# Optimization experiments

Hardware: AMD Instinct MI355X
Metric: run time of the kernel (lower is better)

The kernel has to match this reference:

```python
import jax, jax.numpy as jnp
import numpy as np
from jax import lax

WIN = 7
K1, K2 = 0.01, 0.03
NP_ = WIN * WIN
COV_NORM = NP_ / (NP_ - 1)


def _box_filter(t, w):
    # t: [B, C, H, W] -> valid 7x7 box mean, [B, C, H-6, W-6]
    B, C, H, W = t.shape
    o = lax.conv_general_dilated(
        t.reshape(B * C, 1, H, W), w, window_strides=(1, 1), padding='VALID',
        dimension_numbers=('NCHW', 'OIHW', 'NCHW'))
    return o.reshape(B, C, H - WIN + 1, W - WIN + 1)


def setup_inputs() -> dict:
    key = jax.random.key(0)
    kx, ky = jax.random.split(key)
    X = jax.random.uniform(kx, (32, 3, 512, 512), dtype=jnp.float32)
    Y = jax.random.uniform(ky, (32, 3, 512, 512), dtype=jnp.float32)
    return {"X": X, "Y": Y}


def reference(X, Y):
    data_range = 1.0
    C1 = (K1 * data_range) ** 2
    C2 = (K2 * data_range) ** 2
    w = jnp.full((1, 1, WIN, WIN), 1.0 / NP_, dtype=X.dtype)

    ux = _box_filter(X, w)
    uy = _box_filter(Y, w)
    uxx = _box_filter(X * X, w)
    uyy = _box_filter(Y * Y, w)
    uxy = _box_filter(X * Y, w)

    vx = COV_NORM * (uxx - ux * ux)
    vy = COV_NORM * (uyy - uy * uy)
    vxy = COV_NORM * (uxy - ux * uy)

    A1 = 2 * ux * uy + C1
    A2 = 2 * vxy + C2
    B1 = ux * ux + uy * uy + C1
    B2 = vx + vy + C2
    S = (A1 * A2) / (B1 * B2)
    # reduced=True: per-channel means then mean over channels == global mean
    # (all channels have identical spatial size)
    return 1.0 - jnp.mean(S)
```

## Files before the change

### kernel.cpp

```cpp
#include <hip/hip_runtime.h>


#define WIN   7
#define IW    512
#define IH    512
#define OUTW  506
#define OUTH  506
#define BAND  63
#define NBANDS 9
#define NIMG  96
#define SSIM_C1 1e-4f
#define SSIM_C2 9e-4f
#define INV_NP  (1.0f/49.0f)
#define COV_NORM (49.0f/48.0f)
#define TOTAL_OUT 24579456.0f

__device__ __forceinline__ float ssim_val(float Sx, float Sy, float Sxx,
                                          float Syy, float Sxy) {
    float ux  = Sx  * INV_NP, uy  = Sy  * INV_NP;
    float uxx = Sxx * INV_NP, uyy = Syy * INV_NP, uxy = Sxy * INV_NP;
    float vx  = COV_NORM * (uxx - ux * ux);
    float vy  = COV_NORM * (uyy - uy * uy);
    float vxy = COV_NORM * (uxy - ux * uy);
    float A1 = 2.0f * ux * uy + SSIM_C1;
    float A2 = 2.0f * vxy + SSIM_C2;
    float B1 = ux * ux + uy * uy + SSIM_C1;
    float B2 = vx + vy + SSIM_C2;
    return (A1 * A2) / (B1 * B2);
}

__global__ void ssim_zero(float* acc) {
    if (threadIdx.x == 0) acc[0] = 0.0f;
}

__global__ __launch_bounds__(256) void ssim_main(const float* __restrict__ X,
                                                 const float* __restrict__ Y,
                                                 float* __restrict__ acc) {
    __shared__ float lsx[IW], lsy[IW], lsxx[IW], lsyy[IW], lsxy[IW];
    const int t    = threadIdx.x;
    const int band = blockIdx.x;
    const int img  = blockIdx.y;
    const int r0   = band * BAND;
    const float* Xi = X + (size_t)img * IH * IW;
    const float* Yi = Y + (size_t)img * IH * IW;
    const int c0 = t, c1 = t + 256;

    float rx0[7], ry0[7], rx1[7], ry1[7];
    float sx0 = 0, sy0 = 0, sxx0 = 0, syy0 = 0, sxy0 = 0;
    float sx1 = 0, sy1 = 0, sxx1 = 0, syy1 = 0, sxy1 = 0;

#pragma unroll
    for (int i = 0; i < 6; ++i) {
        int ri = r0 + i;
        float x0 = Xi[ri * IW + c0], y0 = Yi[ri * IW + c0];
        float x1 = Xi[ri * IW + c1], y1 = Yi[ri * IW + c1];
        rx0[i] = x0; ry0[i] = y0; rx1[i] = x1; ry1[i] = y1;
        sx0 += x0; sy0 += y0; sxx0 += x0 * x0; syy0 += y0 * y0; sxy0 += x0 * y0;
        sx1 += x1; sy1 += y1; sxx1 += x1 * x1; syy1 += y1 * y1; sxy1 += x1 * y1;
    }

    float accS = 0.0f;
    int j = 0;
    bool done = false;
    for (int b7 = 0; b7 < BAND / 7; ++b7) {
#pragma unroll
        for (int u = 0; u < 7; ++u, ++j) {
            int r = r0 + j;
            if (r >= OUTH) { done = true; break; }
            int ri = r + 6;
            const int sn = (u + 6) % 7;

            float x0 = Xi[ri * IW + c0], y0 = Yi[ri * IW + c0];
            float x1 = Xi[ri * IW + c1], y1 = Yi[ri * IW + c1];
            sx0 += x0; sy0 += y0; sxx0 += x0 * x0; syy0 += y0 * y0; sxy0 += x0 * y0;
            sx1 += x1; sy1 += y1; sxx1 += x1 * x1; syy1 += y1 * y1; sxy1 += x1 * y1;
            rx0[sn] = x0; ry0[sn] = y0; rx1[sn] = x1; ry1[sn] = y1;

            __syncthreads();
            lsx[c0] = sx0; lsy[c0] = sy0; lsxx[c0] = sxx0; lsyy[c0] = syy0; lsxy[c0] = sxy0;
            lsx[c1] = sx1; lsy[c1] = sy1; lsxx[c1] = sxx1; lsyy[c1] = syy1; lsxy[c1] = sxy1;
            __syncthreads();

            if (t < 253) {
                int oc = 2 * t;
                float aSx = 0, aSy = 0, aSxx = 0, aSyy = 0, aSxy = 0;
#pragma unroll
                for (int k = 0; k < 7; ++k) {
                    aSx  += lsx [oc + k];
                    aSy  += lsy [oc + k];
                    aSxx += lsxx[oc + k];
                    aSyy += lsyy[oc + k];
                    aSxy += lsxy[oc + k];
                }
                accS += ssim_val(aSx, aSy, aSxx, aSyy, aSxy);
                float bSx  = aSx  - lsx [oc] + lsx [oc + 7];
                float bSy  = aSy  - lsy [oc] + lsy [oc + 7];
                float bSxx = aSxx - lsxx[oc] + lsxx[oc + 7];
                float bSyy = aSyy - lsyy[oc] + lsyy[oc + 7];
                float bSxy = aSxy - lsxy[oc] + lsxy[oc + 7];
                accS += ssim_val(bSx, bSy, bSxx, bSyy, bSxy);
            }

            float xo = rx0[u], yo = ry0[u];
            sx0 -= xo; sy0 -= yo; sxx0 -= xo * xo; syy0 -= yo * yo; sxy0 -= xo * yo;
            xo = rx1[u]; yo = ry1[u];
            sx1 -= xo; sy1 -= yo; sxx1 -= xo * xo; syy1 -= yo * yo; sxy1 -= xo * yo;
        }
        if (done) break;
    }

    for (int off = 32; off > 0; off >>= 1)
        accS += __shfl_down(accS, off, 64);
    __shared__ float wsum[4];
    if ((t & 63) == 0) wsum[t >> 6] = accS;
    __syncthreads();
    if (t == 0) atomicAdd(acc, wsum[0] + wsum[1] + wsum[2] + wsum[3]);
}

__global__ void ssim_finalize(const float* __restrict__ acc,
                              float* __restrict__ out) {
    if (threadIdx.x == 0) out[0] = 1.0f - acc[0] / TOTAL_OUT;
}

extern "C" void kernel_launch(void* const* d_in, const int* in_sizes, int n_in,
                              void* d_out, int out_size, void* d_ws, size_t ws_size,
                              hipStream_t stream) {
    const float* X = (const float*)d_in[0];
    const float* Y = (const float*)d_in[1];
    float* acc = (float*)d_ws;
    float* out = (float*)d_out;

    hipLaunchKernelGGL(ssim_zero, dim3(1), dim3(64), 0, stream, acc);
    hipLaunchKernelGGL(ssim_main, dim3(NBANDS, NIMG), dim3(256), 0, stream,
                       X, Y, acc);
    hipLaunchKernelGGL(ssim_finalize, dim3(1), dim3(64), 0, stream, acc, out);
}
```

Measured before the change: 253.6 us.

## Restructure SSIM kernel with float4 rows, per-wave row split and scaled algebra

```diff
diff --git a/kernel.cpp b/kernel.cpp
--- a/kernel.cpp
+++ b/kernel.cpp
@@ -1,120 +1,135 @@
 #include <hip/hip_runtime.h>
 
 
-#define WIN   7
 #define IW    512
-#define IH    512
 #define OUTW  506
 #define OUTH  506
-#define BAND  63
-#define NBANDS 9
+#define BAND  46
+#define NBANDS 11
 #define NIMG  96
-#define SSIM_C1 1e-4f
-#define SSIM_C2 9e-4f
-#define INV_NP  (1.0f/49.0f)
-#define COV_NORM (49.0f/48.0f)
+#define C1N2  0.2401f
+#define C2N2  2.1609f
+#define KA    (49.0f/24.0f)
+#define KB    (49.0f/48.0f)
 #define TOTAL_OUT 24579456.0f
-
-__device__ __forceinline__ float ssim_val(float Sx, float Sy, float Sxx,
-                                          float Syy, float Sxy) {
-    float ux  = Sx  * INV_NP, uy  = Sy  * INV_NP;
-    float uxx = Sxx * INV_NP, uyy = Syy * INV_NP, uxy = Sxy * INV_NP;
-    float vx  = COV_NORM * (uxx - ux * ux);
-    float vy  = COV_NORM * (uyy - uy * uy);
-    float vxy = COV_NORM * (uxy - ux * uy);
-    float A1 = 2.0f * ux * uy + SSIM_C1;
-    float A2 = 2.0f * vxy + SSIM_C2;
-    float B1 = ux * ux + uy * uy + SSIM_C1;
-    float B2 = vx + vy + SSIM_C2;
-    return (A1 * A2) / (B1 * B2);
-}
 
 __global__ void ssim_zero(float* acc) {
     if (threadIdx.x == 0) acc[0] = 0.0f;
 }
 
-__global__ __launch_bounds__(256) void ssim_main(const float* __restrict__ X,
+__global__ __launch_bounds__(128) void ssim_main(const float* __restrict__ X,
                                                  const float* __restrict__ Y,
                                                  float* __restrict__ acc) {
-    __shared__ float lsx[IW], lsy[IW], lsxx[IW], lsyy[IW], lsxy[IW];
+    __shared__ float plane[2][5][65 * 12];
+
     const int t    = threadIdx.x;
     const int band = blockIdx.x;
     const int img  = blockIdx.y;
     const int r0   = band * BAND;
-    const float* Xi = X + (size_t)img * IH * IW;
-    const float* Yi = Y + (size_t)img * IH * IW;
-    const int c0 = t, c1 = t + 256;
+    const float4* X4 = (const float4*)(X + (size_t)img * IW * IW);
+    const float4* Y4 = (const float4*)(Y + (size_t)img * IW * IW);
 
-    float rx0[7], ry0[7], rx1[7], ry1[7];
-    float sx0 = 0, sy0 = 0, sxx0 = 0, syy0 = 0, sxy0 = 0;
-    float sx1 = 0, sy1 = 0, sxx1 = 0, syy1 = 0, sxy1 = 0;
+    float4 s0 = {0,0,0,0}, s1 = {0,0,0,0}, s2 = {0,0,0,0},
+           s3 = {0,0,0,0}, s4 = {0,0,0,0};
 
 #pragma unroll
     for (int i = 0; i < 6; ++i) {
-        int ri = r0 + i;
-        float x0 = Xi[ri * IW + c0], y0 = Yi[ri * IW + c0];
-        float x1 = Xi[ri * IW + c1], y1 = Yi[ri * IW + c1];
-        rx0[i] = x0; ry0[i] = y0; rx1[i] = x1; ry1[i] = y1;
-        sx0 += x0; sy0 += y0; sxx0 += x0 * x0; syy0 += y0 * y0; sxy0 += x0 * y0;
-        sx1 += x1; sy1 += y1; sxx1 += x1 * x1; syy1 += y1 * y1; sxy1 += x1 * y1;
+        float4 x = X4[(r0 + i) * 128 + t];
+        float4 y = Y4[(r0 + i) * 128 + t];
+        s0.x += x.x; s0.y += x.y; s0.z += x.z; s0.w += x.w;
+        s1.x += y.x; s1.y += y.y; s1.z += y.z; s1.w += y.w;
+        s2.x = fmaf(x.x,x.x,s2.x); s2.y = fmaf(x.y,x.y,s2.y);
+        s2.z = fmaf(x.z,x.z,s2.z); s2.w = fmaf(x.w,x.w,s2.w);
+        s3.x = fmaf(y.x,y.x,s3.x); s3.y = fmaf(y.y,y.y,s3.y);
+        s3.z = fmaf(y.z,y.z,s3.z); s3.w = fmaf(y.w,y.w,s3.w);
+        s4.x = fmaf(x.x,y.x,s4.x); s4.y = fmaf(x.y,y.y,s4.y);
+        s4.z = fmaf(x.z,y.z,s4.z); s4.w = fmaf(x.w,y.w,s4.w);
     }
 
+    const int wslot = 12 * (t >> 1) + 4 * (t & 1);
+    const int wv = t >> 6;
+    const int s  = t & 63;
     float accS = 0.0f;
-    int j = 0;
-    bool done = false;
-    for (int b7 = 0; b7 < BAND / 7; ++b7) {
+
+    for (int j = 0; j < BAND; j += 2) {
 #pragma unroll
-        for (int u = 0; u < 7; ++u, ++j) {
-            int r = r0 + j;
-            if (r >= OUTH) { done = true; break; }
-            int ri = r + 6;
-            const int sn = (u + 6) % 7;
+        for (int k = 0; k < 2; ++k) {
+            const int rr = r0 + j + k;
+            float4 x = X4[(rr + 6) * 128 + t];
+            float4 y = Y4[(rr + 6) * 128 + t];
+            s0.x += x.x; s0.y += x.y; s0.z += x.z; s0.w += x.w;
+            s1.x += y.x; s1.y += y.y; s1.z += y.z; s1.w += y.w;
+            s2.x = fmaf(x.x,x.x,s2.x); s2.y = fmaf(x.y,x.y,s2.y);
+            s2.z = fmaf(x.z,x.z,s2.z); s2.w = fmaf(x.w,x.w,s2.w);
+            s3.x = fmaf(y.x,y.x,s3.x); s3.y = fmaf(y.y,y.y,s3.y);
+            s3.z = fmaf(y.z,y.z,s3.z); s3.w = fmaf(y.w,y.w,s3.w);
+            s4.x = fmaf(x.x,y.x,s4.x); s4.y = fmaf(x.y,y.y,s4.y);
+            s4.z = fmaf(x.z,y.z,s4.z); s4.w = fmaf(x.w,y.w,s4.w);
+            *(float4*)&plane[k][0][wslot] = s0;
+            *(float4*)&plane[k][1][wslot] = s1;
+            *(float4*)&plane[k][2][wslot] = s2;
+            *(float4*)&plane[k][3][wslot] = s3;
+            *(float4*)&plane[k][4][wslot] = s4;
+            float4 ox = X4[rr * 128 + t];
+            float4 oy = Y4[rr * 128 + t];
+            s0.x -= ox.x; s0.y -= ox.y; s0.z -= ox.z; s0.w -= ox.w;
+            s1.x -= oy.x; s1.y -= oy.y; s1.z -= oy.z; s1.w -= oy.w;
+            s2.x = fmaf(-ox.x,ox.x,s2.x); s2.y = fmaf(-ox.y,ox.y,s2.y);
+            s2.z = fmaf(-ox.z,ox.z,s2.z); s2.w = fmaf(-ox.w,ox.w,s2.w);
+            s3.x = fmaf(-oy.x,oy.x,s3.x); s3.y = fmaf(-oy.y,oy.y,s3.y);
+            s3.z = fmaf(-oy.z,oy.z,s3.z); s3.w = fmaf(-oy.w,oy.w,s3.w);
+            s4.x = fmaf(-ox.x,oy.x,s4.x); s4.y = fmaf(-ox.y,oy.y,s4.y);
+            s4.z = fmaf(-ox.z,oy.z,s4.z); s4.w = fmaf(-ox.w,oy.w,s4.w);
+        }
+        __syncthreads();
 
-            float x0 = Xi[ri * IW + c0], y0 = Yi[ri * IW + c0];
-            float x1 = Xi[ri * IW + c1], y1 = Yi[ri * IW + c1];
-            sx0 += x0; sy0 += y0; sxx0 += x0 * x0; syy0 += y0 * y0; sxy0 += x0 * y0;
-            sx1 += x1; sy1 += y1; sxx1 += x1 * x1; syy1 += y1 * y1; sxy1 += x1 * y1;
-            rx0[sn] = x0; ry0[sn] = y0; rx1[sn] = x1; ry1[sn] = y1;
-
-            __syncthreads();
-            lsx[c0] = sx0; lsy[c0] = sy0; lsxx[c0] = sxx0; lsyy[c0] = syy0; lsxy[c0] = sxy0;
-            lsx[c1] = sx1; lsy[c1] = sy1; lsxx[c1] = sxx1; lsyy[c1] = syy1; lsxy[c1] = sxy1;
-            __syncthreads();
-
-            if (t < 253) {
-                int oc = 2 * t;
-                float aSx = 0, aSy = 0, aSxx = 0, aSyy = 0, aSxy = 0;
+        float W[5][8];
 #pragma unroll
-                for (int k = 0; k < 7; ++k) {
-                    aSx  += lsx [oc + k];
-                    aSy  += lsy [oc + k];
-                    aSxx += lsxx[oc + k];
-                    aSyy += lsyy[oc + k];
-                    aSxy += lsxy[oc + k];
-                }
-                accS += ssim_val(aSx, aSy, aSxx, aSyy, aSxy);
-                float bSx  = aSx  - lsx [oc] + lsx [oc + 7];
-                float bSy  = aSy  - lsy [oc] + lsy [oc + 7];
-                float bSxx = aSxx - lsxx[oc] + lsxx[oc + 7];
-                float bSyy = aSyy - lsyy[oc] + lsyy[oc + 7];
-                float bSxy = aSxy - lsxy[oc] + lsxy[oc + 7];
-                accS += ssim_val(bSx, bSy, bSxx, bSyy, bSxy);
+        for (int q = 0; q < 5; ++q) {
+            const float* pl = plane[wv][q];
+            float4 a = *(const float4*)(pl + 12 * s);
+            float4 b = *(const float4*)(pl + 12 * s + 4);
+            float4 cc = *(const float4*)(pl + 12 * (s + 1));
+            float2 dd = *(const float2*)(pl + 12 * (s + 1) + 4);
+            float c[14] = {a.x, a.y, a.z, a.w, b.x, b.y, b.z, b.w,
+                           cc.x, cc.y, cc.z, cc.w, dd.x, dd.y};
+            float Wv = ((c[0] + c[1]) + (c[2] + c[3])) +
+                       ((c[4] + c[5]) + c[6]);
+            W[q][0] = Wv;
+#pragma unroll
+            for (int m = 1; m < 8; ++m) {
+                Wv += c[m + 6] - c[m - 1];
+                W[q][m] = Wv;
             }
-
-            float xo = rx0[u], yo = ry0[u];
-            sx0 -= xo; sy0 -= yo; sxx0 -= xo * xo; syy0 -= yo * yo; sxy0 -= xo * yo;
-            xo = rx1[u]; yo = ry1[u];
-            sx1 -= xo; sy1 -= yo; sxx1 -= xo * xo; syy1 -= yo * yo; sxy1 -= xo * yo;
         }
-        if (done) break;
+#pragma unroll
+        for (int m = 0; m < 8; ++m) {
+            float Sx = W[0][m], Sy = W[1][m];
+            float Sxx = W[2][m], Syy = W[3][m], Sxy = W[4][m];
+            float sxsy = Sx * Sy;
+            float p    = fmaf(Sx, Sx, Sy * Sy);
+            float a1   = fmaf(2.0f, sxsy, C1N2);
+            float b1   = p + C1N2;
+            float t1   = fmaf(49.0f, Sxy, -sxsy);
+            float a2   = fmaf(KA, t1, C2N2);
+            float qq   = Sxx + Syy;
+            float t2   = fmaf(49.0f, qq, -p);
+            float b2   = fmaf(KB, t2, C2N2);
+            float num  = a1 * a2;
+            float den  = b1 * b2;
+            float S    = num * __builtin_amdgcn_rcpf(den);
+            accS += (8 * s + m < OUTW) ? S : 0.0f;
+        }
+        __syncthreads();
     }
 
+#pragma unroll
     for (int off = 32; off > 0; off >>= 1)
         accS += __shfl_down(accS, off, 64);
-    __shared__ float wsum[4];
-    if ((t & 63) == 0) wsum[t >> 6] = accS;
+    __shared__ float wsum[2];
+    if (s == 0) wsum[wv] = accS;
     __syncthreads();
-    if (t == 0) atomicAdd(acc, wsum[0] + wsum[1] + wsum[2] + wsum[3]);
+    if (t == 0) atomicAdd(acc, wsum[0] + wsum[1]);
 }
 
 __global__ void ssim_finalize(const float* __restrict__ acc,
@@ -127,11 +142,11 @@
                               hipStream_t stream) {
     const float* X = (const float*)d_in[0];
     const float* Y = (const float*)d_in[1];
-    float* acc = (float*)d_ws;
+    float* accum = (float*)d_ws;
     float* out = (float*)d_out;
 
-    hipLaunchKernelGGL(ssim_zero, dim3(1), dim3(64), 0, stream, acc);
-    hipLaunchKernelGGL(ssim_main, dim3(NBANDS, NIMG), dim3(256), 0, stream,
-                       X, Y, acc);
-    hipLaunchKernelGGL(ssim_finalize, dim3(1), dim3(64), 0, stream, acc, out);
+    hipLaunchKernelGGL(ssim_zero, dim3(1), dim3(64), 0, stream, accum);
+    hipLaunchKernelGGL(ssim_main, dim3(NBANDS, NIMG), dim3(128), 0, stream,
+                       X, Y, accum);
+    hipLaunchKernelGGL(ssim_finalize, dim3(1), dim3(64), 0, stream, accum, out);
 }
```

New measurement: 248.5 us. 1.02x faster.
